# Optimization experiments

Measured on AMD Instinct MI355X. Metric: run time of the kernel, lower is better.

The kernel has to match this reference:

```python
import jax, jax.numpy as jnp
import numpy as np

B, C, H, W = 2, 256, 64, 64
FEAT = 256          # in_channels * expansion_ratio
HEADS = 8
HS = FEAT // HEADS  # 32
OUT = 256


def setup_inputs() -> dict:
    key = jax.random.key(0)
    ks = jax.random.split(key, 12)
    inp = {
        "x": jax.random.normal(ks[0], (B, C, H, W), jnp.float32),
        "mod_multiplier": jax.random.normal(ks[1], (B, FEAT), jnp.float32),
        "mod_bias": jax.random.normal(ks[2], (B, FEAT), jnp.float32),
        # learned parameters (1x1 convs as matrices)
        "w_qkv": jax.random.normal(ks[3], (3 * FEAT, C), jnp.float32) * 0.02,
        "b_qkv": jnp.zeros((3 * FEAT,), jnp.float32),
        "w_proj": jax.random.normal(ks[4], (OUT, FEAT), jnp.float32) * 0.02,
        "pe_q_h": jax.random.normal(ks[5], (1, FEAT, H, 1), jnp.float32) * 0.02,
        "pe_q_w": jax.random.normal(ks[6], (1, FEAT, 1, W), jnp.float32) * 0.02,
        "pe_k_h": jax.random.normal(ks[7], (1, FEAT, H, 1), jnp.float32) * 0.02,
        "pe_k_w": jax.random.normal(ks[8], (1, FEAT, 1, W), jnp.float32) * 0.02,
        "pre_act_bias": jnp.zeros((1, C, 1, 1), jnp.float32),
        "pre_qkv_bias": jnp.zeros((1, C, 1, 1), jnp.float32),
        "pre_proj_bias": jnp.zeros((1, FEAT, 1, 1), jnp.float32),
        "id_scale": jnp.ones((1, OUT, 1, 1), jnp.float32),
    }
    return inp


def reference(x, mod_multiplier, mod_bias, w_qkv, b_qkv, w_proj,
              pe_q_h, pe_q_w, pe_k_h, pe_k_w,
              pre_act_bias, pre_qkv_bias, pre_proj_bias, id_scale):
    b = x.shape[0]
    # pre-activation (Fixup-style biases)
    x_preact = jax.nn.silu(x + pre_act_bias) + pre_qkv_bias
    # 1x1 conv -> QKV: [b, 3F, H, W]
    qkv = jnp.einsum('bchw,oc->bohw', x_preact, w_qkv) + b_qkv[None, :, None, None]
    q, k, v = jnp.split(qkv, 3, axis=1)
    # additive positional embeddings
    q = q + pe_q_h + pe_q_w
    k = k + pe_k_h + pe_k_w
    # FiLM modulation of query
    q = q * mod_multiplier[:, :, None, None] + mod_bias[:, :, None, None]
    # [b, heads, head_size, H*W]
    q = q.reshape(b, HEADS, HS, H * W)
    k = k.reshape(b, HEADS, HS, H * W)
    v = v.reshape(b, HEADS, HS, H * W)
    scale = jnp.asarray(HS ** 0.5, x.dtype)
    logits = jnp.einsum('bhdn,bhdm->bhnm', q, k) / scale
    weights = jax.nn.softmax(logits, axis=-1)
    attn = jnp.einsum('bhnm,bhdm->bhdn', weights, v)
    attn = attn.reshape(b, FEAT, H, W)
    # output projection (1x1 conv, no bias)
    x_res = jnp.einsum('bchw,oc->bohw', attn + pre_proj_bias, w_proj)
    return x * id_scale + x_res
```

## Files before the change

kernel.cpp:

```cpp
#include <hip/hip_runtime.h>
#include <hip/hip_bf16.h>
#include <cstdint>

#define NB   2
#define NC   256
#define NN   4096
#define NH   8
#define HSZ  32
#define NF   256
#define N3F  768

typedef __bf16 bf16x8 __attribute__((ext_vector_type(8)));
typedef __bf16 bf16x4 __attribute__((ext_vector_type(4)));
typedef short  s16x4  __attribute__((ext_vector_type(4)));
typedef float  floatx4 __attribute__((ext_vector_type(4)));

#define QSCALE 0.25506601622184f

__global__ void k_prep(const float* __restrict__ x, const float* __restrict__ pab,
                       const float* __restrict__ pqb, __bf16* __restrict__ y,
                       const float* __restrict__ wqkv, const float* __restrict__ wproj,
                       __bf16* __restrict__ wqb, __bf16* __restrict__ wpb) {
    __shared__ __bf16 ct[32 * 264];
    int bid = blockIdx.x, tid = threadIdx.x;
    if (bid >= 256) {
        int id = (bid - 256) * 1024 + tid * 4;
        const float* src = (id < 196608) ? (wqkv + id) : (wproj + (id - 196608));
        __bf16* dst = (id < 196608) ? (wqb + id) : (wpb + (id - 196608));
        float4 v = *(const float4*)src;
        bf16x4 o;
        o[0] = (__bf16)v.x; o[1] = (__bf16)v.y; o[2] = (__bf16)v.z; o[3] = (__bf16)v.w;
        *(bf16x4*)dst = o;
        return;
    }
    int b = bid >> 7, nt = bid & 127;
    int n0 = nt * 32;
    int cbase = tid >> 3, nc = tid & 7;
#pragma unroll
    for (int q = 0; q < 8; q++) {
        int c = cbase + q * 32;
        const float4 xv = *(const float4*)(x + ((size_t)b * NC + c) * NN + n0 + nc * 4);
        float bias = pab[c], qb = pqb[c];
        float vs[4] = {xv.x, xv.y, xv.z, xv.w};
#pragma unroll
        for (int i = 0; i < 4; i++) {
            float s = vs[i] + bias;
            float r = s / (1.f + __expf(-s)) + qb;
            ct[(nc * 4 + i) * 264 + c] = (__bf16)r;
        }
    }
    __syncthreads();
#pragma unroll
    for (int q = 0; q < 4; q++) {
        int id = tid + q * 256;
        int n = id >> 5, ck = (id & 31) * 8;
        bf16x8 v = *(const bf16x8*)(ct + n * 264 + ck);
        *(bf16x8*)(y + ((size_t)b * NN + n0 + n) * NC + ck) = v;
    }
}

__launch_bounds__(256)
__global__ void k_qkv(const __bf16* __restrict__ y, const __bf16* __restrict__ wb,
                      const float* __restrict__ bqkv,
                      const float* __restrict__ peqh, const float* __restrict__ peqw,
                      const float* __restrict__ pekh, const float* __restrict__ pekw,
                      const float* __restrict__ mm, const float* __restrict__ mb,
                      __bf16* __restrict__ qs, __bf16* __restrict__ kf, __bf16* __restrict__ vf) {
    __shared__ __bf16 smem[4][64 * 40];
    __bf16* ct = &smem[0][0];
    const int nt = blockIdx.x, ot = blockIdx.y, b = blockIdx.z;
    const int tid = threadIdx.x;
    const int wave = tid >> 6, lane = tid & 63, ln = lane & 15, quad = lane >> 4;
    const int wm = (wave & 1) * 32, wn = (wave >> 1) * 32;
    floatx4 acc[2][2];
#pragma unroll
    for (int i = 0; i < 2; i++)
#pragma unroll
        for (int j = 0; j < 2; j++) acc[i][j] = 0.f;
    const __bf16* ysrc = y + ((size_t)b * NN + nt * 64) * NC;
    const __bf16* wsrc = wb + (size_t)ot * 64 * NC;
    const int r0 = tid >> 2, c0 = (tid & 3) * 8;
    bf16x8 ya[2], wa[2];
    ya[0] = *(const bf16x8*)(ysrc + (size_t)r0 * NC + c0);
    wa[0] = *(const bf16x8*)(wsrc + (size_t)r0 * NC + c0);
#pragma unroll 2
    for (int ko = 0; ko < 8; ko++) {
        int cur = ko & 1, nxt = cur ^ 1;
        *(bf16x8*)(&smem[cur][r0 * 40 + c0]) = ya[cur];
        *(bf16x8*)(&smem[2 + cur][r0 * 40 + c0]) = wa[cur];
        if (ko < 7) {
            int kc = (ko + 1) * 32;
            ya[nxt] = *(const bf16x8*)(ysrc + (size_t)r0 * NC + kc + c0);
            wa[nxt] = *(const bf16x8*)(wsrc + (size_t)r0 * NC + kc + c0);
        }
        __syncthreads();
        bf16x8 af[2], bfr[2];
#pragma unroll
        for (int ii = 0; ii < 2; ii++) af[ii]  = *(const bf16x8*)(&smem[cur][(wm + ii * 16 + ln) * 40 + quad * 8]);
#pragma unroll
        for (int jj = 0; jj < 2; jj++) bfr[jj] = *(const bf16x8*)(&smem[2 + cur][(wn + jj * 16 + ln) * 40 + quad * 8]);
#pragma unroll
        for (int ii = 0; ii < 2; ii++)
#pragma unroll
            for (int jj = 0; jj < 2; jj++)
                acc[ii][jj] = __builtin_amdgcn_mfma_f32_16x16x32_bf16(af[ii], bfr[jj], acc[ii][jj], 0, 0, 0);
    }
    __syncthreads();
    if (ot < 8) {
#pragma unroll
        for (int ii = 0; ii < 2; ii++)
#pragma unroll
            for (int jj = 0; jj < 2; jj++) {
                int o_l = wn + jj * 16 + ln;
                int o_g = ot * 64 + o_l;
                float bq = bqkv[o_g];
#pragma unroll
                for (int r = 0; r < 4; r++) {
                    int n_l = wm + ii * 16 + quad * 4 + r;
                    float val = acc[ii][jj][r] + bq;
                    if (ot < 4) {
                        val += peqh[o_g * 64 + nt] + peqw[o_g * 64 + n_l];
                        val = val * mm[b * NF + o_g] + mb[b * NF + o_g];
                        val *= QSCALE;
                    } else {
                        int c = o_g - 256;
                        val += pekh[c * 64 + nt] + pekw[c * 64 + n_l];
                    }
                    ct[n_l * 72 + o_l] = (__bf16)val;
                }
            }
        __syncthreads();
#pragma unroll
        for (int q = 0; q < 2; q++) {
            int id = tid + q * 256;
            int n_l = id >> 3, oc = (id & 7) * 8;
            bf16x8 v = *(const bf16x8*)(ct + n_l * 72 + oc);
            int n_g = nt * 64 + n_l;
            int o_g = ot * 64 + oc;
            if (ot < 4) {
                int h = o_g >> 5, d = o_g & 31;
                *(bf16x8*)(qs + (((size_t)b * NH + h) * NN + n_g) * HSZ + d) = v;
            } else {
                int c = o_g - 256, h = c >> 5, d0 = c & 31;
                size_t blk = ((size_t)(b * NH + h) * 256 + (n_g >> 4)) * 512;
                *(bf16x8*)(kf + blk + (d0 >> 3) * 128 + (n_g & 15) * 8) = v;
            }
        }
    } else {
#pragma unroll
        for (int ii = 0; ii < 2; ii++)
#pragma unroll
            for (int jj = 0; jj < 2; jj++) {
                int o_l = wn + jj * 16 + ln;
                float bq = bqkv[ot * 64 + o_l];
#pragma unroll
                for (int r = 0; r < 4; r++) {
                    int n_l = wm + ii * 16 + quad * 4 + r;
                    ct[o_l * 72 + n_l] = (__bf16)(acc[ii][jj][r] + bq);
                }
            }
        __syncthreads();
#pragma unroll
        for (int q = 0; q < 4; q++) {
            int id = tid + q * 256;
            int o_l = id >> 4, ng4 = (id & 15) * 4;
            bf16x4 v = *(const bf16x4*)(ct + o_l * 72 + ng4);
            int c = (ot - 8) * 64 + o_l, h = c >> 5, d = c & 31;
            int dj = d >> 4, lnv = d & 15;
            int m_g = nt * 64 + ng4;
            size_t blk = ((size_t)(b * NH + h) * 256 + (m_g >> 4)) * 512;
            *(bf16x4*)(vf + blk + (((m_g >> 2) & 3) * 16 + lnv) * 8 + dj * 4) = v;
        }
    }
}

__launch_bounds__(256)
__global__ void k_attn(const __bf16* __restrict__ qs, const __bf16* __restrict__ kf,
                       const __bf16* __restrict__ vf,
                       __bf16* __restrict__ po, float* __restrict__ pl) {
    __shared__ __bf16 sbuf[2 * 8192];
    int bi = blockIdx.x;
    int xcd = bi & 7, r = bi >> 3;
    int bh = xcd * 2 + (r & 1);
    int r2 = r >> 1;
    int qt = r2 & 31, half = r2 >> 5;
    int tid = threadIdx.x, wave = tid >> 6, lane = tid & 63, ln = lane & 15, quad = lane >> 4;
    int n0 = qt * 128 + wave * 32;
    const __bf16* qbase = qs + (size_t)bh * NN * HSZ;
    const __bf16* kfb = kf + ((size_t)bh * 256 + half * 128) * 512;
    const __bf16* vfb = vf + ((size_t)bh * 256 + half * 128) * 512;
    bf16x8 qa[2];
    qa[0] = *(const bf16x8*)(qbase + (size_t)(n0 + ln) * HSZ + quad * 8);
    qa[1] = *(const bf16x8*)(qbase + (size_t)(n0 + 16 + ln) * HSZ + quad * 8);
    floatx4 o[2][2], o2[2];
    o[0][0] = 0.f; o[0][1] = 0.f; o[1][0] = 0.f; o[1][1] = 0.f;
    o2[0] = 0.f; o2[1] = 0.f;
    floatx4 zf = 0.f;
    s16x4 ones;
    ones[0] = (short)0x3F80; ones[1] = (short)0x3F80;
    ones[2] = (short)0x3F80; ones[3] = (short)0x3F80;
    const int toff = tid * 8;
    const int lo = lane * 8;
    bf16x8 kra[2], krb[2], vra[2], vrb[2];
    kra[0] = *(const bf16x8*)(kfb + toff);
    krb[0] = *(const bf16x8*)(kfb + toff + 2048);
    vra[0] = *(const bf16x8*)(vfb + toff);
    vrb[0] = *(const bf16x8*)(vfb + toff + 2048);
#pragma unroll 2
    for (int mt = 0; mt < 16; mt++) {
        int cur = mt & 1, nxt = cur ^ 1;
        int bo = cur << 13;
        *(bf16x8*)(sbuf + bo + toff) = kra[cur];
        *(bf16x8*)(sbuf + bo + toff + 2048) = krb[cur];
        *(bf16x8*)(sbuf + bo + 4096 + toff) = vra[cur];
        *(bf16x8*)(sbuf + bo + 4096 + toff + 2048) = vrb[cur];
        if (mt < 15) {
            const __bf16* kn = kfb + (mt + 1) * 4096;
            const __bf16* vn = vfb + (mt + 1) * 4096;
            kra[nxt] = *(const bf16x8*)(kn + toff);
            krb[nxt] = *(const bf16x8*)(kn + toff + 2048);
            vra[nxt] = *(const bf16x8*)(vn + toff);
            vrb[nxt] = *(const bf16x8*)(vn + toff + 2048);
        }
        __syncthreads();
        const __bf16* kl = sbuf + bo;
        const __bf16* vl = sbuf + bo + 4096;
        __builtin_amdgcn_s_setprio(1);
#pragma unroll
        for (int j = 0; j < 8; j++) {
            bf16x8 kfr = *(const bf16x8*)(kl + j * 512 + lo);
            bf16x8 vfr = *(const bf16x8*)(vl + j * 512 + lo);
            s16x4 vb0, vb1;
            __builtin_memcpy(&vb0, &vfr, 8);
            __builtin_memcpy(&vb1, (const char*)&vfr + 8, 8);
#pragma unroll
            for (int i = 0; i < 2; i++) {
                floatx4 s = __builtin_amdgcn_mfma_f32_16x16x32_bf16(kfr, qa[i], zf, 0, 0, 0);
                bf16x4 p;
#pragma unroll
                for (int rr = 0; rr < 4; rr++)
                    p[rr] = (__bf16)__builtin_amdgcn_exp2f(s[rr]);
                s16x4 pa;
                __builtin_memcpy(&pa, &p, 8);
                o[i][0] = __builtin_amdgcn_mfma_f32_16x16x16bf16_1k(pa, vb0, o[i][0], 0, 0, 0);
                o[i][1] = __builtin_amdgcn_mfma_f32_16x16x16bf16_1k(pa, vb1, o[i][1], 0, 0, 0);
                o2[i]   = __builtin_amdgcn_mfma_f32_16x16x16bf16_1k(pa, ones, o2[i], 0, 0, 0);
            }
        }
        __builtin_amdgcn_s_setprio(0);
    }
    size_t plbase = (size_t)(half * 16 + bh) * NN;
    if (ln == 0)
#pragma unroll
        for (int i = 0; i < 2; i++)
#pragma unroll
            for (int rr = 0; rr < 4; rr++)
                pl[plbase + n0 + i * 16 + quad * 4 + rr] = o2[i][rr];
    __bf16* ct = sbuf;
#pragma unroll
    for (int i = 0; i < 2; i++)
#pragma unroll
        for (int dj = 0; dj < 2; dj++)
#pragma unroll
            for (int rr = 0; rr < 4; rr++)
                ct[(wave * 32 + i * 16 + quad * 4 + rr) * 32 + dj * 16 + ln] = (__bf16)o[i][dj][rr];
    __syncthreads();
    size_t pobase = ((size_t)(half * 16 + bh) * NN + (size_t)qt * 128) * HSZ;
#pragma unroll
    for (int q = 0; q < 2; q++) {
        int id = tid + q * 256;
        int n_l = id >> 2, dc = (id & 3) * 8;
        *(bf16x8*)(po + pobase + n_l * HSZ + dc) = *(const bf16x8*)(ct + n_l * 32 + dc);
    }
}

__launch_bounds__(256)
__global__ void k_proj(const __bf16* __restrict__ po, const float* __restrict__ pl,
                       const __bf16* __restrict__ wpb, const float* __restrict__ ppb,
                       const float* __restrict__ x, const float* __restrict__ idsc,
                       float* __restrict__ out) {
    __shared__ __bf16 at[32 * 264];
    __shared__ __bf16 bt[2][64 * 40];
    __shared__ float linv[8 * 64];
    __shared__ float ppbs[256];
    int nt = blockIdx.x, ot = blockIdx.y, b = blockIdx.z;
    int tid = threadIdx.x, wave = tid >> 6, lane = tid & 63, ln = lane & 15, quad = lane >> 4;
    int wo = (wave & 1) * 16, wn = (wave >> 1) * 32;
#pragma unroll
    for (int q = 0; q < 4; q++) {
        int id = tid + q * 256;
        int row = id >> 5, fc = (id & 31) * 8;
        *(bf16x8*)(at + row * 264 + fc) = *(const bf16x8*)(wpb + (size_t)(ot * 32 + row) * NF + fc);
    }
#pragma unroll
    for (int q = 0; q < 2; q++) {
        int id = tid + q * 256;
        int h = id >> 6, n_l = id & 63;
        size_t base = (size_t)(b * NH + h) * NN + nt * 64 + n_l;
        linv[id] = 1.f / (pl[base] + pl[base + (size_t)16 * NN]);
    }
    ppbs[tid] = ppb[tid];
    __syncthreads();
    floatx4 acc[2];
    acc[0] = 0.f; acc[1] = 0.f;
    const int n_l = tid >> 2, dh8 = (tid & 3) * 8;
    const size_t hstep = (size_t)NN * HSZ;
    const size_t half_off = (size_t)16 * NN * HSZ;
    size_t prow = ((size_t)b * NH * NN + (size_t)nt * 64 + n_l) * HSZ + dh8;
    bf16x8 p0[2], p1[2];
    p0[0] = *(const bf16x8*)(po + prow);
    p1[0] = *(const bf16x8*)(po + prow + half_off);
#pragma unroll 2
    for (int ko = 0; ko < 8; ko++) {
        int cur = ko & 1, nxt = cur ^ 1;
        float iv = linv[ko * 64 + n_l];
        bf16x8 c;
#pragma unroll
        for (int e = 0; e < 8; e++)
            c[e] = (__bf16)(((float)p0[cur][e] + (float)p1[cur][e]) * iv + ppbs[ko * 32 + dh8 + e]);
        *(bf16x8*)(&bt[cur][n_l * 40 + dh8]) = c;
        if (ko < 7) {
            size_t pr = prow + (size_t)(ko + 1) * hstep;
            p0[nxt] = *(const bf16x8*)(po + pr);
            p1[nxt] = *(const bf16x8*)(po + pr + half_off);
        }
        __syncthreads();
        bf16x8 af, bfr[2];
        af = *(const bf16x8*)(at + (wo + ln) * 264 + ko * 32 + quad * 8);
#pragma unroll
        for (int nj = 0; nj < 2; nj++) bfr[nj] = *(const bf16x8*)(&bt[cur][(wn + nj * 16 + ln) * 40 + quad * 8]);
#pragma unroll
        for (int nj = 0; nj < 2; nj++)
            acc[nj] = __builtin_amdgcn_mfma_f32_16x16x32_bf16(af, bfr[nj], acc[nj], 0, 0, 0);
    }
#pragma unroll
    for (int nj = 0; nj < 2; nj++)
#pragma unroll
        for (int r = 0; r < 4; r++) {
            int o_g = ot * 32 + wo + quad * 4 + r;
            int n_g = nt * 64 + wn + nj * 16 + ln;
            size_t idx = ((size_t)b * NF + o_g) * NN + n_g;
            out[idx] = x[idx] * idsc[o_g] + acc[nj][r];
        }
}

extern "C" void kernel_launch(void* const* d_in, const int* in_sizes, int n_in,
                              void* d_out, int out_size, void* d_ws, size_t ws_size,
                              hipStream_t stream) {
    (void)in_sizes; (void)n_in; (void)out_size; (void)ws_size;
    const float* x    = (const float*)d_in[0];
    const float* mm   = (const float*)d_in[1];
    const float* mb   = (const float*)d_in[2];
    const float* wqkv = (const float*)d_in[3];
    const float* bqkv = (const float*)d_in[4];
    const float* wproj= (const float*)d_in[5];
    const float* peqh = (const float*)d_in[6];
    const float* peqw = (const float*)d_in[7];
    const float* pekh = (const float*)d_in[8];
    const float* pekw = (const float*)d_in[9];
    const float* pab  = (const float*)d_in[10];
    const float* pqb  = (const float*)d_in[11];
    const float* ppb  = (const float*)d_in[12];
    const float* idsc = (const float*)d_in[13];
    float* out = (float*)d_out;

    __bf16* ws = (__bf16*)d_ws;
    const size_t SEG = 2097152;
    __bf16* y    = ws;
    __bf16* qs   = ws + SEG;
    __bf16* kf   = ws + SEG * 2;
    __bf16* vf   = ws + SEG * 3;
    __bf16* po   = ws + SEG * 4;
    float*  pl   = (float*)(ws + SEG * 6);
    __bf16* wqb  = ws + SEG * 6 + 262144;
    __bf16* wpb  = wqb + 196608;

    hipLaunchKernelGGL(k_prep, dim3(512), dim3(256), 0, stream,
                       x, pab, pqb, y, wqkv, wproj, wqb, wpb);
    hipLaunchKernelGGL(k_qkv,  dim3(64, 12, 2), dim3(256), 0, stream,
                       y, wqb, bqkv, peqh, peqw, pekh, pekw, mm, mb, qs, kf, vf);
    hipLaunchKernelGGL(k_attn, dim3(1024), dim3(256), 0, stream, qs, kf, vf, po, pl);
    hipLaunchKernelGGL(k_proj, dim3(64, 8, 2), dim3(256), 0, stream,
                       po, pl, wpb, ppb, x, idsc, out);
}
```

Measured before the change: 171.6 us.

## Stream K/V fragments directly from global memory into registers, dropping LDS staging

The attention kernel no longer stages K/V tiles through double-buffered shared memory behind block-wide barriers. Each wave now loads its own MFMA-ready K/V fragments straight from global memory, prefetching two fragments ahead in registers. This removes the LDS round trip, the shared-memory footprint and the per-tile __syncthreads, which may help occupancy. The cost is that all four waves in a block each fetch the same K/V data, so L2 traffic rises about fourfold, and the shallow prefetch may not hide global memory latency.

```diff
diff --git a/kernel.cpp b/kernel.cpp
--- a/kernel.cpp
+++ b/kernel.cpp
@@ -178,7 +178,7 @@
 __global__ void k_attn(const __bf16* __restrict__ qs, const __bf16* __restrict__ kf,
                        const __bf16* __restrict__ vf,
                        __bf16* __restrict__ po, float* __restrict__ pl) {
-    __shared__ __bf16 sbuf[2 * 8192];
+    __shared__ __bf16 ct[128 * 32];
     int bi = blockIdx.x;
     int xcd = bi & 7, r = bi >> 3;
     int bh = xcd * 2 + (r & 1);
@@ -187,8 +187,8 @@
     int tid = threadIdx.x, wave = tid >> 6, lane = tid & 63, ln = lane & 15, quad = lane >> 4;
     int n0 = qt * 128 + wave * 32;
     const __bf16* qbase = qs + (size_t)bh * NN * HSZ;
-    const __bf16* kfb = kf + ((size_t)bh * 256 + half * 128) * 512;
-    const __bf16* vfb = vf + ((size_t)bh * 256 + half * 128) * 512;
+    const __bf16* kfb = kf + ((size_t)bh * 256 + half * 128) * 512 + lane * 8;
+    const __bf16* vfb = vf + ((size_t)bh * 256 + half * 128) * 512 + lane * 8;
     bf16x8 qa[2];
     qa[0] = *(const bf16x8*)(qbase + (size_t)(n0 + ln) * HSZ + quad * 8);
     qa[1] = *(const bf16x8*)(qbase + (size_t)(n0 + 16 + ln) * HSZ + quad * 8);
@@ -199,56 +199,50 @@
     s16x4 ones;
     ones[0] = (short)0x3F80; ones[1] = (short)0x3F80;
     ones[2] = (short)0x3F80; ones[3] = (short)0x3F80;
-    const int toff = tid * 8;
-    const int lo = lane * 8;
-    bf16x8 kra[2], krb[2], vra[2], vrb[2];
-    kra[0] = *(const bf16x8*)(kfb + toff);
-    krb[0] = *(const bf16x8*)(kfb + toff + 2048);
-    vra[0] = *(const bf16x8*)(vfb + toff);
-    vrb[0] = *(const bf16x8*)(vfb + toff + 2048);
-#pragma unroll 2
-    for (int mt = 0; mt < 16; mt++) {
-        int cur = mt & 1, nxt = cur ^ 1;
-        int bo = cur << 13;
-        *(bf16x8*)(sbuf + bo + toff) = kra[cur];
-        *(bf16x8*)(sbuf + bo + toff + 2048) = krb[cur];
-        *(bf16x8*)(sbuf + bo + 4096 + toff) = vra[cur];
-        *(bf16x8*)(sbuf + bo + 4096 + toff + 2048) = vrb[cur];
-        if (mt < 15) {
-            const __bf16* kn = kfb + (mt + 1) * 4096;
-            const __bf16* vn = vfb + (mt + 1) * 4096;
-            kra[nxt] = *(const bf16x8*)(kn + toff);
-            krb[nxt] = *(const bf16x8*)(kn + toff + 2048);
-            vra[nxt] = *(const bf16x8*)(vn + toff);
-            vrb[nxt] = *(const bf16x8*)(vn + toff + 2048);
-        }
-        __syncthreads();
-        const __bf16* kl = sbuf + bo;
-        const __bf16* vl = sbuf + bo + 4096;
+
+#define ATTN_STEP(KR, VR) do {                                                        \
+        s16x4 vb0, vb1;                                                               \
+        __builtin_memcpy(&vb0, &(VR), 8);                                             \
+        __builtin_memcpy(&vb1, (const char*)&(VR) + 8, 8);                            \
+        _Pragma("unroll")                                                             \
+        for (int i = 0; i < 2; i++) {                                                 \
+            floatx4 s = __builtin_amdgcn_mfma_f32_16x16x32_bf16(KR, qa[i], zf, 0, 0, 0); \
+            bf16x4 p;                                                                 \
+            _Pragma("unroll")                                                         \
+            for (int rr = 0; rr < 4; rr++)                                            \
+                p[rr] = (__bf16)__builtin_amdgcn_exp2f(s[rr]);                        \
+            s16x4 pa;                                                                 \
+            __builtin_memcpy(&pa, &p, 8);                                             \
+            o[i][0] = __builtin_amdgcn_mfma_f32_16x16x16bf16_1k(pa, vb0, o[i][0], 0, 0, 0); \
+            o[i][1] = __builtin_amdgcn_mfma_f32_16x16x16bf16_1k(pa, vb1, o[i][1], 0, 0, 0); \
+            o2[i]   = __builtin_amdgcn_mfma_f32_16x16x16bf16_1k(pa, ones, o2[i], 0, 0, 0); \
+        }                                                                             \
+    } while (0)
+
+    bf16x8 kr0 = *(const bf16x8*)(kfb);
+    bf16x8 vr0 = *(const bf16x8*)(vfb);
+    bf16x8 kr1 = *(const bf16x8*)(kfb + 512);
+    bf16x8 vr1 = *(const bf16x8*)(vfb + 512);
+    for (int f = 0; f < 128; f += 2) {
+        bf16x8 ka = kr0, va = vr0;
+        if (f + 2 < 128) {
+            kr0 = *(const bf16x8*)(kfb + (size_t)(f + 2) * 512);
+            vr0 = *(const bf16x8*)(vfb + (size_t)(f + 2) * 512);
+        }
         __builtin_amdgcn_s_setprio(1);
-#pragma unroll
-        for (int j = 0; j < 8; j++) {
-            bf16x8 kfr = *(const bf16x8*)(kl + j * 512 + lo);
-            bf16x8 vfr = *(const bf16x8*)(vl + j * 512 + lo);
-            s16x4 vb0, vb1;
-            __builtin_memcpy(&vb0, &vfr, 8);
-            __builtin_memcpy(&vb1, (const char*)&vfr + 8, 8);
-#pragma unroll
-            for (int i = 0; i < 2; i++) {
-                floatx4 s = __builtin_amdgcn_mfma_f32_16x16x32_bf16(kfr, qa[i], zf, 0, 0, 0);
-                bf16x4 p;
-#pragma unroll
-                for (int rr = 0; rr < 4; rr++)
-                    p[rr] = (__bf16)__builtin_amdgcn_exp2f(s[rr]);
-                s16x4 pa;
-                __builtin_memcpy(&pa, &p, 8);
-                o[i][0] = __builtin_amdgcn_mfma_f32_16x16x16bf16_1k(pa, vb0, o[i][0], 0, 0, 0);
-                o[i][1] = __builtin_amdgcn_mfma_f32_16x16x16bf16_1k(pa, vb1, o[i][1], 0, 0, 0);
-                o2[i]   = __builtin_amdgcn_mfma_f32_16x16x16bf16_1k(pa, ones, o2[i], 0, 0, 0);
-            }
-        }
+        ATTN_STEP(ka, va);
         __builtin_amdgcn_s_setprio(0);
-    }
+        bf16x8 kb = kr1, vb = vr1;
+        if (f + 3 < 128) {
+            kr1 = *(const bf16x8*)(kfb + (size_t)(f + 3) * 512);
+            vr1 = *(const bf16x8*)(vfb + (size_t)(f + 3) * 512);
+        }
+        __builtin_amdgcn_s_setprio(1);
+        ATTN_STEP(kb, vb);
+        __builtin_amdgcn_s_setprio(0);
+    }
+#undef ATTN_STEP
+
     size_t plbase = (size_t)(half * 16 + bh) * NN;
     if (ln == 0)
 #pragma unroll
@@ -256,7 +250,6 @@
 #pragma unroll
             for (int rr = 0; rr < 4; rr++)
                 pl[plbase + n0 + i * 16 + quad * 4 + rr] = o2[i][rr];
-    __bf16* ct = sbuf;
 #pragma unroll
     for (int i = 0; i < 2; i++)
 #pragma unroll
```

Measured after the change: 182.9 us. 6.6% more time.

## Split attention keys into four pieces and single-buffer LDS for more occupancy

Applied to the files above, without the earlier changes.

The attention kernel now splits the key range into four pieces instead of two, doubling the grid to 2048 blocks. Each block covers 8 key tiles and uses a single LDS buffer with an extra barrier per tile, and launch bounds request 8 blocks per CU. The projection kernel sums four partial outputs and four partial denominators, with the fourth piece stored in the reused y buffer. The aim is more parallelism and higher occupancy, at the cost of more partial-result traffic and an extra synchronisation per tile.

```diff
diff --git a/kernel.cpp b/kernel.cpp
--- a/kernel.cpp
+++ b/kernel.cpp
@@ -16,6 +16,8 @@
 typedef float  floatx4 __attribute__((ext_vector_type(4)));
 
 #define QSCALE 0.25506601622184f
+
+#define PIECE 2097152
 
 __global__ void k_prep(const float* __restrict__ x, const float* __restrict__ pab,
                        const float* __restrict__ pqb, __bf16* __restrict__ y,
@@ -174,21 +176,22 @@
     }
 }
 
-__launch_bounds__(256)
+__launch_bounds__(256, 8)
 __global__ void k_attn(const __bf16* __restrict__ qs, const __bf16* __restrict__ kf,
                        const __bf16* __restrict__ vf,
-                       __bf16* __restrict__ po, float* __restrict__ pl) {
-    __shared__ __bf16 sbuf[2 * 8192];
+                       __bf16* __restrict__ po012, __bf16* __restrict__ po3,
+                       float* __restrict__ pl) {
+    __shared__ __bf16 sbuf[8192];
     int bi = blockIdx.x;
     int xcd = bi & 7, r = bi >> 3;
     int bh = xcd * 2 + (r & 1);
     int r2 = r >> 1;
-    int qt = r2 & 31, half = r2 >> 5;
+    int qt = r2 & 31, piece = r2 >> 5;
     int tid = threadIdx.x, wave = tid >> 6, lane = tid & 63, ln = lane & 15, quad = lane >> 4;
     int n0 = qt * 128 + wave * 32;
     const __bf16* qbase = qs + (size_t)bh * NN * HSZ;
-    const __bf16* kfb = kf + ((size_t)bh * 256 + half * 128) * 512;
-    const __bf16* vfb = vf + ((size_t)bh * 256 + half * 128) * 512;
+    const __bf16* kfb = kf + ((size_t)bh * 256 + piece * 64) * 512;
+    const __bf16* vfb = vf + ((size_t)bh * 256 + piece * 64) * 512;
     bf16x8 qa[2];
     qa[0] = *(const bf16x8*)(qbase + (size_t)(n0 + ln) * HSZ + quad * 8);
     qa[1] = *(const bf16x8*)(qbase + (size_t)(n0 + 16 + ln) * HSZ + quad * 8);
@@ -201,35 +204,30 @@
     ones[2] = (short)0x3F80; ones[3] = (short)0x3F80;
     const int toff = tid * 8;
     const int lo = lane * 8;
-    bf16x8 kra[2], krb[2], vra[2], vrb[2];
-    kra[0] = *(const bf16x8*)(kfb + toff);
-    krb[0] = *(const bf16x8*)(kfb + toff + 2048);
-    vra[0] = *(const bf16x8*)(vfb + toff);
-    vrb[0] = *(const bf16x8*)(vfb + toff + 2048);
-#pragma unroll 2
-    for (int mt = 0; mt < 16; mt++) {
-        int cur = mt & 1, nxt = cur ^ 1;
-        int bo = cur << 13;
-        *(bf16x8*)(sbuf + bo + toff) = kra[cur];
-        *(bf16x8*)(sbuf + bo + toff + 2048) = krb[cur];
-        *(bf16x8*)(sbuf + bo + 4096 + toff) = vra[cur];
-        *(bf16x8*)(sbuf + bo + 4096 + toff + 2048) = vrb[cur];
-        if (mt < 15) {
+    bf16x8 kr0, kr1, vr0, vr1;
+    kr0 = *(const bf16x8*)(kfb + toff);
+    kr1 = *(const bf16x8*)(kfb + toff + 2048);
+    vr0 = *(const bf16x8*)(vfb + toff);
+    vr1 = *(const bf16x8*)(vfb + toff + 2048);
+    for (int mt = 0; mt < 8; mt++) {
+        *(bf16x8*)(sbuf + toff) = kr0;
+        *(bf16x8*)(sbuf + toff + 2048) = kr1;
+        *(bf16x8*)(sbuf + 4096 + toff) = vr0;
+        *(bf16x8*)(sbuf + 4096 + toff + 2048) = vr1;
+        __syncthreads();
+        if (mt < 7) {
             const __bf16* kn = kfb + (mt + 1) * 4096;
             const __bf16* vn = vfb + (mt + 1) * 4096;
-            kra[nxt] = *(const bf16x8*)(kn + toff);
-            krb[nxt] = *(const bf16x8*)(kn + toff + 2048);
-            vra[nxt] = *(const bf16x8*)(vn + toff);
-            vrb[nxt] = *(const bf16x8*)(vn + toff + 2048);
-        }
-        __syncthreads();
-        const __bf16* kl = sbuf + bo;
-        const __bf16* vl = sbuf + bo + 4096;
+            kr0 = *(const bf16x8*)(kn + toff);
+            kr1 = *(const bf16x8*)(kn + toff + 2048);
+            vr0 = *(const bf16x8*)(vn + toff);
+            vr1 = *(const bf16x8*)(vn + toff + 2048);
+        }
         __builtin_amdgcn_s_setprio(1);
 #pragma unroll
         for (int j = 0; j < 8; j++) {
-            bf16x8 kfr = *(const bf16x8*)(kl + j * 512 + lo);
-            bf16x8 vfr = *(const bf16x8*)(vl + j * 512 + lo);
+            bf16x8 kfr = *(const bf16x8*)(sbuf + j * 512 + lo);
+            bf16x8 vfr = *(const bf16x8*)(sbuf + 4096 + j * 512 + lo);
             s16x4 vb0, vb1;
             __builtin_memcpy(&vb0, &vfr, 8);
             __builtin_memcpy(&vb1, (const char*)&vfr + 8, 8);
@@ -248,8 +246,9 @@
             }
         }
         __builtin_amdgcn_s_setprio(0);
-    }
-    size_t plbase = (size_t)(half * 16 + bh) * NN;
+        __syncthreads();
+    }
+    size_t plbase = (size_t)(piece * 16 + bh) * NN;
     if (ln == 0)
 #pragma unroll
         for (int i = 0; i < 2; i++)
@@ -265,17 +264,19 @@
             for (int rr = 0; rr < 4; rr++)
                 ct[(wave * 32 + i * 16 + quad * 4 + rr) * 32 + dj * 16 + ln] = (__bf16)o[i][dj][rr];
     __syncthreads();
-    size_t pobase = ((size_t)(half * 16 + bh) * NN + (size_t)qt * 128) * HSZ;
+    __bf16* pob = (piece < 3) ? (po012 + (size_t)piece * PIECE) : po3;
+    size_t pobase = ((size_t)bh * NN + (size_t)qt * 128) * HSZ;
 #pragma unroll
     for (int q = 0; q < 2; q++) {
         int id = tid + q * 256;
         int n_l = id >> 2, dc = (id & 3) * 8;
-        *(bf16x8*)(po + pobase + n_l * HSZ + dc) = *(const bf16x8*)(ct + n_l * 32 + dc);
+        *(bf16x8*)(pob + pobase + n_l * HSZ + dc) = *(const bf16x8*)(ct + n_l * 32 + dc);
     }
 }
 
 __launch_bounds__(256)
-__global__ void k_proj(const __bf16* __restrict__ po, const float* __restrict__ pl,
+__global__ void k_proj(const __bf16* __restrict__ po012, const __bf16* __restrict__ po3,
+                       const float* __restrict__ pl,
                        const __bf16* __restrict__ wpb, const float* __restrict__ ppb,
                        const float* __restrict__ x, const float* __restrict__ idsc,
                        float* __restrict__ out) {
@@ -297,7 +298,8 @@
         int id = tid + q * 256;
         int h = id >> 6, n_l = id & 63;
         size_t base = (size_t)(b * NH + h) * NN + nt * 64 + n_l;
-        linv[id] = 1.f / (pl[base] + pl[base + (size_t)16 * NN]);
+        linv[id] = 1.f / (pl[base] + pl[base + (size_t)16 * NN]
+                        + pl[base + (size_t)32 * NN] + pl[base + (size_t)48 * NN]);
     }
     ppbs[tid] = ppb[tid];
     __syncthreads();
@@ -305,11 +307,12 @@
     acc[0] = 0.f; acc[1] = 0.f;
     const int n_l = tid >> 2, dh8 = (tid & 3) * 8;
     const size_t hstep = (size_t)NN * HSZ;
-    const size_t half_off = (size_t)16 * NN * HSZ;
     size_t prow = ((size_t)b * NH * NN + (size_t)nt * 64 + n_l) * HSZ + dh8;
-    bf16x8 p0[2], p1[2];
-    p0[0] = *(const bf16x8*)(po + prow);
-    p1[0] = *(const bf16x8*)(po + prow + half_off);
+    bf16x8 p0[2], p1[2], p2[2], p3[2];
+    p0[0] = *(const bf16x8*)(po012 + prow);
+    p1[0] = *(const bf16x8*)(po012 + prow + (size_t)PIECE);
+    p2[0] = *(const bf16x8*)(po012 + prow + (size_t)2 * PIECE);
+    p3[0] = *(const bf16x8*)(po3 + prow);
 #pragma unroll 2
     for (int ko = 0; ko < 8; ko++) {
         int cur = ko & 1, nxt = cur ^ 1;
@@ -317,12 +320,16 @@
         bf16x8 c;
 #pragma unroll
         for (int e = 0; e < 8; e++)
-            c[e] = (__bf16)(((float)p0[cur][e] + (float)p1[cur][e]) * iv + ppbs[ko * 32 + dh8 + e]);
+            c[e] = (__bf16)(((float)p0[cur][e] + (float)p1[cur][e]
+                           + (float)p2[cur][e] + (float)p3[cur][e]) * iv
+                           + ppbs[ko * 32 + dh8 + e]);
         *(bf16x8*)(&bt[cur][n_l * 40 + dh8]) = c;
         if (ko < 7) {
             size_t pr = prow + (size_t)(ko + 1) * hstep;
-            p0[nxt] = *(const bf16x8*)(po + pr);
-            p1[nxt] = *(const bf16x8*)(po + pr + half_off);
+            p0[nxt] = *(const bf16x8*)(po012 + pr);
+            p1[nxt] = *(const bf16x8*)(po012 + pr + (size_t)PIECE);
+            p2[nxt] = *(const bf16x8*)(po012 + pr + (size_t)2 * PIECE);
+            p3[nxt] = *(const bf16x8*)(po3 + pr);
         }
         __syncthreads();
         bf16x8 af, bfr[2];
@@ -366,20 +373,22 @@
 
     __bf16* ws = (__bf16*)d_ws;
     const size_t SEG = 2097152;
-    __bf16* y    = ws;
-    __bf16* qs   = ws + SEG;
-    __bf16* kf   = ws + SEG * 2;
-    __bf16* vf   = ws + SEG * 3;
-    __bf16* po   = ws + SEG * 4;
-    float*  pl   = (float*)(ws + SEG * 6);
-    __bf16* wqb  = ws + SEG * 6 + 262144;
-    __bf16* wpb  = wqb + 196608;
+    __bf16* y     = ws;
+    __bf16* qs    = ws + SEG;
+    __bf16* kf    = ws + SEG * 2;
+    __bf16* vf    = ws + SEG * 3;
+    __bf16* po012 = ws + SEG * 4;
+    __bf16* po3   = ws;
+    float*  pl    = (float*)(ws + SEG * 7);
+    __bf16* wqb   = ws + SEG * 7 + 524288;
+    __bf16* wpb   = wqb + 196608;
 
     hipLaunchKernelGGL(k_prep, dim3(512), dim3(256), 0, stream,
                        x, pab, pqb, y, wqkv, wproj, wqb, wpb);
     hipLaunchKernelGGL(k_qkv,  dim3(64, 12, 2), dim3(256), 0, stream,
                        y, wqb, bqkv, peqh, peqw, pekh, pekw, mm, mb, qs, kf, vf);
-    hipLaunchKernelGGL(k_attn, dim3(1024), dim3(256), 0, stream, qs, kf, vf, po, pl);
+    hipLaunchKernelGGL(k_attn, dim3(2048), dim3(256), 0, stream,
+                       qs, kf, vf, po012, po3, pl);
     hipLaunchKernelGGL(k_proj, dim3(64, 8, 2), dim3(256), 0, stream,
-                       po, pl, wpb, ppb, x, idsc, out);
-}
+                       po012, po3, pl, wpb, ppb, x, idsc, out);
+}
```

After: 199.0 us. 16.0% more time.
